# Optimization experiments

Measured on AMD Instinct MI355X. Metric: run time of the kernel, lower is better.

Reference implementation:

```python
import jax, jax.numpy as jnp
import numpy as np

B, N, D, H, O, K, N_USER, C = 1, 4096, 64, 4, 64, 2, 4000, 2


def setup_inputs() -> dict:
    key = jax.random.key(0)
    ks = jax.random.split(key, 7)
    h = jax.random.normal(ks[0], (B, N, D), jnp.float32)
    # dense 0/1 adjacency per heterogeneous kind, with self-loops so no row is empty
    adj = jax.random.randint(ks[1], (K, B, N, N), 0, 2).astype(jnp.float32)
    hadj = jnp.maximum(adj, jnp.eye(N, dtype=jnp.float32))
    s = 1.0 / np.sqrt(D).astype(np.float32)
    w = jax.random.normal(ks[2], (K, H, D, O), jnp.float32) * s
    a_src = jax.random.normal(ks[3], (K, H, O, 1), jnp.float32) * (1.0 / np.sqrt(O).astype(np.float32))
    a_dst = jax.random.normal(ks[4], (K, H, O, 1), jnp.float32) * (1.0 / np.sqrt(O).astype(np.float32))
    fc_w = jax.random.normal(ks[5], (C, O * K), jnp.float32) * (1.0 / np.sqrt(O * K).astype(np.float32))
    fc_b = jnp.zeros((C,), jnp.float32)
    return {"h": h, "hadj": hadj, "w": w, "a_src": a_src, "a_dst": a_dst, "fc_w": fc_w, "fc_b": fc_b}


def _gat(h, adj, w_k, a_src_k, a_dst_k):
    # h: (B,N,D); adj: (B,N,N); w_k: (H,D,O); a_*: (H,O,1)
    h_prime = jnp.einsum('bnf,hfo->bhno', h, w_k)          # (B,H,N,O)
    t = jnp.tanh(h_prime)
    attn_src = jnp.einsum('bhno,hoi->bhni', t, a_src_k)    # (B,H,N,1)
    attn_dst = jnp.einsum('bhno,hoi->bhni', t, a_dst_k)    # (B,H,N,1)
    attn = attn_src + jnp.swapaxes(attn_dst, -1, -2)       # (B,H,N,N) broadcast add
    attn = jnp.where(attn >= 0, attn, 0.2 * attn)          # LeakyReLU(0.2)
    attn = jnp.where(adj[:, None] > 0, attn, -jnp.inf)     # dense mask
    attn = jax.nn.softmax(attn, axis=-1)                   # dropout is a no-op in eval
    out = jnp.einsum('bhnm,bhmo->bhno', attn, h_prime)     # (B,H,N,O)
    return out.mean(axis=1)                                # mean over heads -> (B,N,O)


def reference(h, hadj, w, a_src, a_dst, fc_w, fc_b):
    embs = []
    for k in range(K):  # small fixed loop over heterogeneous node kinds
        x = _gat(h, hadj[k], w[k], a_src[k], a_dst[k])
        embs.append(x[:, :N_USER])
    type_aware = jnp.concatenate(embs, axis=-1)            # (B, N_USER, K*O)
    logits = type_aware @ fc_w.T + fc_b                    # (B, N_USER, C)
    return jax.nn.log_softmax(logits, axis=-1)
```

## Files before the change

### kernel.cpp

```cpp
#include <hip/hip_runtime.h>
#include <math.h>

constexpr int KK = 2;
constexpr int HH = 4;
constexpr int NN = 4096;
constexpr int DD = 64;
constexpr int OO = 64;
constexpr int NU = 4000;
constexpr int CC = 2;
constexpr int JSPLIT = 4;
constexpr int JCHUNK = NN / JSPLIT;
constexpr float LOG2E = 1.44269504088896340736f;

typedef float vf4 __attribute__((ext_vector_type(4)));

__device__ __forceinline__ float fexp2(float x) {
#if __has_builtin(__builtin_amdgcn_exp2f)
  return __builtin_amdgcn_exp2f(x);
#else
  return exp2f(x);
#endif
}
__device__ __forceinline__ float frcp(float x) {
#if __has_builtin(__builtin_amdgcn_rcpf)
  return __builtin_amdgcn_rcpf(x);
#else
  return 1.0f / x;
#endif
}
__device__ __forceinline__ float ftanh(float x) {
  float e = fexp2(x * (2.0f * LOG2E));
  return 1.0f - 2.0f * frcp(e + 1.0f);
}

__global__ __launch_bounds__(256) void gat_phase1(
    const float* __restrict__ hsrc, const float* __restrict__ w,
    const float* __restrict__ a_src, const float* __restrict__ a_dst,
    const float* __restrict__ fc_w,
    float* __restrict__ src_s, float* __restrict__ att_d,
    float* __restrict__ att_g0, float* __restrict__ att_g1) {
  const int kh = blockIdx.y;
  const int k = kh >> 2;
  const int i0 = blockIdx.x * 64;
  const int tid = threadIdx.x;

  __shared__ float h_s[DD][68];
  __shared__ float w_s[DD][OO];

  {
    const float4* wp = (const float4*)(w + (size_t)kh * DD * OO);
    float4* ws4 = (float4*)w_s;
    for (int t = tid; t < DD * OO / 4; t += 256) ws4[t] = wp[t];
  }
  for (int t = tid; t < 1024; t += 256) {
    const int row = t >> 4;
    const int f4 = (t & 15) * 4;
    float4 v = *(const float4*)(hsrc + (size_t)(i0 + row) * DD + f4);
    h_s[f4 + 0][row] = v.x;
    h_s[f4 + 1][row] = v.y;
    h_s[f4 + 2][row] = v.z;
    h_s[f4 + 3][row] = v.w;
  }
  __syncthreads();

  const int og = tid & 15;
  const int rg = tid >> 4;
  const int o0 = og * 4;
  const int r0 = rg * 4;

  float hp[4][4];
#pragma unroll
  for (int j = 0; j < 4; ++j)
#pragma unroll
    for (int u = 0; u < 4; ++u) hp[j][u] = 0.0f;

#pragma unroll 8
  for (int f = 0; f < DD; ++f) {
    float4 hv = *(const float4*)&h_s[f][r0];
    float4 wv = *(const float4*)&w_s[f][o0];
    hp[0][0] = fmaf(hv.x, wv.x, hp[0][0]);
    hp[0][1] = fmaf(hv.x, wv.y, hp[0][1]);
    hp[0][2] = fmaf(hv.x, wv.z, hp[0][2]);
    hp[0][3] = fmaf(hv.x, wv.w, hp[0][3]);
    hp[1][0] = fmaf(hv.y, wv.x, hp[1][0]);
    hp[1][1] = fmaf(hv.y, wv.y, hp[1][1]);
    hp[1][2] = fmaf(hv.y, wv.z, hp[1][2]);
    hp[1][3] = fmaf(hv.y, wv.w, hp[1][3]);
    hp[2][0] = fmaf(hv.z, wv.x, hp[2][0]);
    hp[2][1] = fmaf(hv.z, wv.y, hp[2][1]);
    hp[2][2] = fmaf(hv.z, wv.z, hp[2][2]);
    hp[2][3] = fmaf(hv.z, wv.w, hp[2][3]);
    hp[3][0] = fmaf(hv.w, wv.x, hp[3][0]);
    hp[3][1] = fmaf(hv.w, wv.y, hp[3][1]);
    hp[3][2] = fmaf(hv.w, wv.z, hp[3][2]);
    hp[3][3] = fmaf(hv.w, wv.w, hp[3][3]);
  }

  float as[4], ad[4], f0[4], f1[4];
#pragma unroll
  for (int u = 0; u < 4; ++u) {
    as[u] = a_src[kh * OO + o0 + u];
    ad[u] = a_dst[kh * OO + o0 + u];
    f0[u] = fc_w[0 * (KK * OO) + k * OO + o0 + u];
    f1[u] = fc_w[1 * (KK * OO) + k * OO + o0 + u];
  }

#pragma unroll
  for (int j = 0; j < 4; ++j) {
    float sp = 0.0f, dp = 0.0f, g0 = 0.0f, g1 = 0.0f;
#pragma unroll
    for (int u = 0; u < 4; ++u) {
      float v = hp[j][u];
      float t = ftanh(v);
      sp = fmaf(t, as[u], sp);
      dp = fmaf(t, ad[u], dp);
      g0 = fmaf(v, f0[u], g0);
      g1 = fmaf(v, f1[u], g1);
    }
#pragma unroll
    for (int off = 1; off < 16; off <<= 1) {
      sp += __shfl_xor(sp, off, 64);
      dp += __shfl_xor(dp, off, 64);
      g0 += __shfl_xor(g0, off, 64);
      g1 += __shfl_xor(g1, off, 64);
    }
    if (og == 0) {
      const int i = i0 + r0 + j;
      src_s[kh * NN + i] = sp * LOG2E;
      att_d[kh * NN + i] = dp * LOG2E;
      att_g0[kh * NN + i] = g0;
      att_g1[kh * NN + i] = g1;
    }
  }
}

__global__ __launch_bounds__(256) void gat_phase2(
    const float* __restrict__ adj, const float* __restrict__ src_s,
    const float* __restrict__ att_d, const float* __restrict__ att_g0,
    const float* __restrict__ att_g1, float* __restrict__ P) {
  const int k = blockIdx.y >> 2;
  const int chunk = blockIdx.y & 3;
  const int r0 = blockIdx.x * 16;
  const int tid = threadIdx.x;
  const int wave = tid >> 6;
  const int lane = tid & 63;
  const int row = lane & 15;
  const int jsub = lane >> 4;
  const int i = r0 + row;

  float sreg[4];
#pragma unroll
  for (int h = 0; h < 4; ++h) sreg[h] = src_s[(k * HH + h) * NN + i];

  float l[4], a0[4], a1[4];
#pragma unroll
  for (int h = 0; h < 4; ++h) {
    l[h] = 0.0f;
    a0[h] = 0.0f;
    a1[h] = 0.0f;
  }

  const float* adjrow = adj + (size_t)k * NN * NN + (size_t)i * NN;
  const int jbase = chunk * JCHUNK + jsub * 4;

#pragma unroll 2
  for (int t = wave; t < JCHUNK / 16; t += 4) {
    const int jb = jbase + t * 16;
    vf4 av = *(const vf4*)(adjrow + jb);
#pragma unroll
    for (int h = 0; h < 4; ++h) {
      const size_t pb = (size_t)(k * HH + h) * NN + jb;
      vf4 dv = *(const vf4*)(att_d + pb);
      vf4 g0v = *(const vf4*)(att_g0 + pb);
      vf4 g1v = *(const vf4*)(att_g1 + pb);
#pragma unroll
      for (int jj = 0; jj < 4; ++jj) {
        float s = sreg[h] + dv[jj];
        float sl = fmaxf(s, 0.2f * s);
        float p = av[jj] * fexp2(sl);
        l[h] += p;
        a0[h] = fmaf(p, g0v[jj], a0[h]);
        a1[h] = fmaf(p, g1v[jj], a1[h]);
      }
    }
  }

#pragma unroll
  for (int h = 0; h < 4; ++h) {
    l[h] += __shfl_xor(l[h], 16, 64);
    l[h] += __shfl_xor(l[h], 32, 64);
    a0[h] += __shfl_xor(a0[h], 16, 64);
    a0[h] += __shfl_xor(a0[h], 32, 64);
    a1[h] += __shfl_xor(a1[h], 16, 64);
    a1[h] += __shfl_xor(a1[h], 32, 64);
  }

  __shared__ float sred[4][12][16];
  if (lane < 16) {
#pragma unroll
    for (int h = 0; h < 4; ++h) {
      sred[wave][h * 3 + 0][row] = l[h];
      sred[wave][h * 3 + 1][row] = a0[h];
      sred[wave][h * 3 + 2][row] = a1[h];
    }
  }
  __syncthreads();
  if (tid < 192) {
    const int v = tid >> 4;
    const int rr = tid & 15;
    float sum = sred[0][v][rr] + sred[1][v][rr] + sred[2][v][rr] + sred[3][v][rr];
    const int h = v / 3, c = v % 3;
    size_t base = ((((size_t)(k * JSPLIT + chunk) * HH + h) * 3 + c)) * NU + (r0 + rr);
    P[base] = sum;
  }
}

__global__ __launch_bounds__(256) void gat_phase3(
    const float* __restrict__ P, const float* __restrict__ fc_b,
    float* __restrict__ out) {
  const int i = blockIdx.x * 256 + threadIdx.x;
  if (i >= NU) return;
  float l0 = fc_b[0], l1 = fc_b[1];
#pragma unroll
  for (int k = 0; k < KK; ++k) {
#pragma unroll
    for (int q = 0; q < HH; ++q) {
      float ls = 0.0f, a0 = 0.0f, a1 = 0.0f;
#pragma unroll
      for (int ch = 0; ch < JSPLIT; ++ch) {
        size_t b = (((size_t)(k * JSPLIT + ch) * HH + q) * 3) * NU + i;
        ls += P[b];
        a0 += P[b + NU];
        a1 += P[b + 2 * (size_t)NU];
      }
      float inv = 1.0f / ls;
      l0 = fmaf(0.25f * a0, inv, l0);
      l1 = fmaf(0.25f * a1, inv, l1);
    }
  }
  float m = fmaxf(l0, l1);
  float lse = m + logf(expf(l0 - m) + expf(l1 - m));
  out[i * CC + 0] = l0 - lse;
  out[i * CC + 1] = l1 - lse;
}

extern "C" void kernel_launch(void* const* d_in, const int* in_sizes, int n_in,
                              void* d_out, int out_size, void* d_ws, size_t ws_size,
                              hipStream_t stream) {
  const float* hsrc  = (const float*)d_in[0];
  const float* hadj  = (const float*)d_in[1];
  const float* w     = (const float*)d_in[2];
  const float* a_src = (const float*)d_in[3];
  const float* a_dst = (const float*)d_in[4];
  const float* fc_w  = (const float*)d_in[5];
  const float* fc_b  = (const float*)d_in[6];
  float* out = (float*)d_out;

  char* ws = (char*)d_ws;
  float* src_s  = (float*)(ws + 0 * 131072);
  float* att_d  = (float*)(ws + 1 * 131072);
  float* att_g0 = (float*)(ws + 2 * 131072);
  float* att_g1 = (float*)(ws + 3 * 131072);
  float* P      = (float*)(ws + 4 * 131072);

  dim3 g1(NN / 64, KK * HH);
  gat_phase1<<<g1, 256, 0, stream>>>(hsrc, w, a_src, a_dst, fc_w,
                                     src_s, att_d, att_g0, att_g1);
  dim3 g2(NU / 16, KK * JSPLIT);
  gat_phase2<<<g2, 256, 0, stream>>>(hadj, src_s, att_d, att_g0, att_g1, P);
  gat_phase3<<<(NU + 255) / 256, 256, 0, stream>>>(P, fc_b, out);
}
```

Before: 265.2 us.

## Stage per-column attention terms in LDS, double the j split, prefetch adjacency rows

Phase 2 now stages the att_d, att_g0 and att_g1 chunk for all heads into shared memory once per block, so these terms no longer come from global memory or L2 on every tile. JSPLIT goes from 4 to 8, which doubles the grid and halves the per-block column range. The adjacency loads are software-pipelined with a two-deep register prefetch over a fully unrolled loop. The costs are about 24KB of LDS per block, which can limit occupancy, and twice as many partial sums written to P. Phase 3 picks up the new JSPLIT through the shared constant.

```diff
diff --git a/kernel.cpp b/kernel.cpp
--- a/kernel.cpp
+++ b/kernel.cpp
@@ -8,8 +8,9 @@
 constexpr int OO = 64;
 constexpr int NU = 4000;
 constexpr int CC = 2;
-constexpr int JSPLIT = 4;
+constexpr int JSPLIT = 8;
 constexpr int JCHUNK = NN / JSPLIT;
+constexpr int NTILE = JCHUNK / 16;
 constexpr float LOG2E = 1.44269504088896340736f;
 
 typedef float vf4 __attribute__((ext_vector_type(4)));
@@ -138,8 +139,8 @@
     const float* __restrict__ adj, const float* __restrict__ src_s,
     const float* __restrict__ att_d, const float* __restrict__ att_g0,
     const float* __restrict__ att_g1, float* __restrict__ P) {
-  const int k = blockIdx.y >> 2;
-  const int chunk = blockIdx.y & 3;
+  const int k = blockIdx.y >> 3;
+  const int chunk = blockIdx.y & 7;
   const int r0 = blockIdx.x * 16;
   const int tid = threadIdx.x;
   const int wave = tid >> 6;
@@ -147,6 +148,21 @@
   const int row = lane & 15;
   const int jsub = lane >> 4;
   const int i = r0 + row;
+  const int j0 = chunk * JCHUNK;
+
+  __shared__ float lds_att[12][JCHUNK];
+  {
+    const float* planes[3] = {att_d, att_g0, att_g1};
+#pragma unroll
+    for (int step = 0; step < 6; ++step) {
+      const int fi = step * 256 + tid;
+      const int v = fi >> 7;
+      const int pos = (fi & 127) * 4;
+      const int p = v >> 2, h = v & 3;
+      vf4 val = *(const vf4*)(planes[p] + (size_t)(k * HH + h) * NN + j0 + pos);
+      *(vf4*)&lds_att[v][pos] = val;
+    }
+  }
 
   float sreg[4];
 #pragma unroll
@@ -160,23 +176,28 @@
     a1[h] = 0.0f;
   }
 
-  const float* adjrow = adj + (size_t)k * NN * NN + (size_t)i * NN;
-  const int jbase = chunk * JCHUNK + jsub * 4;
-
-#pragma unroll 2
-  for (int t = wave; t < JCHUNK / 16; t += 4) {
-    const int jb = jbase + t * 16;
-    vf4 av = *(const vf4*)(adjrow + jb);
+  __syncthreads();
+
+  const float* arow = adj + (size_t)k * NN * NN + (size_t)i * NN + j0 + jsub * 4;
+  vf4 apre0 = *(const vf4*)(arow + (wave + 0) * 16);
+  vf4 apre1 = *(const vf4*)(arow + (wave + 4) * 16);
+
+#pragma unroll
+  for (int s = 0; s < 8; ++s) {
+    const int t = wave + s * 4;
+    const vf4 av = apre0;
+    apre0 = apre1;
+    if (s < 6) apre1 = *(const vf4*)(arow + (t + 8) * 16);
+    const int jloc = jsub * 4 + t * 16;
 #pragma unroll
     for (int h = 0; h < 4; ++h) {
-      const size_t pb = (size_t)(k * HH + h) * NN + jb;
-      vf4 dv = *(const vf4*)(att_d + pb);
-      vf4 g0v = *(const vf4*)(att_g0 + pb);
-      vf4 g1v = *(const vf4*)(att_g1 + pb);
+      vf4 dv = *(const vf4*)&lds_att[0 * 4 + h][jloc];
+      vf4 g0v = *(const vf4*)&lds_att[1 * 4 + h][jloc];
+      vf4 g1v = *(const vf4*)&lds_att[2 * 4 + h][jloc];
 #pragma unroll
       for (int jj = 0; jj < 4; ++jj) {
-        float s = sreg[h] + dv[jj];
-        float sl = fmaxf(s, 0.2f * s);
+        float s2 = sreg[h] + dv[jj];
+        float sl = fmaxf(s2, 0.2f * s2);
         float p = av[jj] * fexp2(sl);
         l[h] += p;
         a0[h] = fmaf(p, g0v[jj], a0[h]);
@@ -208,9 +229,11 @@
   if (tid < 192) {
     const int v = tid >> 4;
     const int rr = tid & 15;
-    float sum = sred[0][v][rr] + sred[1][v][rr] + sred[2][v][rr] + sred[3][v][rr];
+    float sum =
+        sred[0][v][rr] + sred[1][v][rr] + sred[2][v][rr] + sred[3][v][rr];
     const int h = v / 3, c = v % 3;
-    size_t base = ((((size_t)(k * JSPLIT + chunk) * HH + h) * 3 + c)) * NU + (r0 + rr);
+    size_t base =
+        ((((size_t)(k * JSPLIT + chunk) * HH + h) * 3 + c)) * NU + (r0 + rr);
     P[base] = sum;
   }
 }
```

Result: faster. 222.7 us (-16.0%).
